# Performance work log

Hardware: AMD Instinct MI355X
Metric: run time of the kernel (lower is better)

The kernel has to match this reference:

```python
import jax, jax.numpy as jnp
import numpy as np

N_U = 50000
N_V = 50000
E = 640000
D = 128  # u_dim == v_dim == hid_dim (required for shape consistency)


def setup_inputs() -> dict:
    key = jax.random.key(0)
    ks = jax.random.split(key, 12)
    scale = 1.0 / np.sqrt(D)
    return {
        "X_u": jax.random.normal(ks[0], (N_U, D), dtype=jnp.float32),
        "X_v": jax.random.normal(ks[1], (N_V, D), dtype=jnp.float32),
        "edge_u": jax.random.randint(ks[2], (E,), 0, N_U, dtype=jnp.int32),
        "edge_v": jax.random.randint(ks[3], (E,), 0, N_V, dtype=jnp.int32),
        "W0": jax.random.uniform(ks[4], (D, D), jnp.float32, -scale, scale),
        "b0": jax.random.uniform(ks[5], (D,), jnp.float32, -scale, scale),
        "W1": jax.random.uniform(ks[6], (D, D), jnp.float32, -scale, scale),
        "b1": jax.random.uniform(ks[7], (D,), jnp.float32, -scale, scale),
        "W2": jax.random.uniform(ks[8], (D, D), jnp.float32, -scale, scale),
        "b2": jax.random.uniform(ks[9], (D,), jnp.float32, -scale, scale),
    }


def reference(X_u, X_v, edge_u, edge_v, W0, b0, W1, b1, W2, b2):
    # bipartite scatter-sum aggregations over the edge list
    def v2u(X):  # X: [N_V, D] -> [N_U, D]
        return jax.ops.segment_sum(X[edge_v], edge_u, num_segments=N_U)

    def u2v(X):  # X: [N_U, D] -> [N_V, D]
        return jax.ops.segment_sum(X[edge_u], edge_v, num_segments=N_V)

    # layer 0 (even): Linear(v_dim->hid) on X_v, then v2u sum
    last_X_u = v2u(X_v @ W0 + b0)
    # layer 1 (odd): Linear(u_dim->hid) on last_X_u, then u2v sum
    last_X_v = u2v(last_X_u @ W1 + b1)
    # layer 2 (even): Linear(v_dim->hid) on last_X_v, then v2u sum
    last_X_u = v2u(last_X_v @ W2 + b2)
    return last_X_u
```

## Files before the change

### kernel.cpp

```cpp
#include <hip/hip_runtime.h>

#define D 128
#define NROW 50000
#define NEDGE 640000
#define CAP 64

#define RBLK 160
#define EPB  4000
#define NBKT 196
#define CELL 64

typedef __attribute__((ext_vector_type(8))) short short8;
typedef __attribute__((ext_vector_type(4))) float f32x4;

__device__ __forceinline__ unsigned short f2bf(float f) {
    unsigned u = __float_as_uint(f);
    unsigned r = (u + 0x7fff + ((u >> 16) & 1)) >> 16;
    return (unsigned short)r;
}
__device__ __forceinline__ void acc2(float& e, float& o, unsigned g) {
    e += __uint_as_float(g << 16);
    o += __uint_as_float(g & 0xffff0000u);
}

__global__ __launch_bounds__(256) void route_cvt_gemm1(const int* __restrict__ eu,
                                                       const int* __restrict__ ev,
                                                       unsigned int* __restrict__ recbuf_u,
                                                       int* __restrict__ counts_u,
                                                       unsigned int* __restrict__ recbuf_v,
                                                       int* __restrict__ counts_v,
                                                       const float4* __restrict__ Xv4,
                                                       ushort4* __restrict__ Xb4,
                                                       const float* __restrict__ W0,
                                                       const float* __restrict__ b0,
                                                       const float* __restrict__ b1,
                                                       const float* __restrict__ W1,
                                                       float* __restrict__ T) {
    const int blk = blockIdx.x, tid = threadIdx.x;
    if (blk < 65) {
        __shared__ float R[2][128];
        int sub = tid >> 7, j = tid & 127;
        int i = blk * 2 + sub;
        bool valid = (i < 130);
        const float* row = nullptr;
        if (valid && i < 128) row = W0 + i * D;
        else if (valid && i == 128) row = b0;
        R[sub][j] = row ? row[j] : 0.f;
        __syncthreads();
        if (!valid) return;
        if (i == 129) { T[129 * D + j] = b1[j]; return; }
        float acc = 0.f;
#pragma unroll 8
        for (int k = 0; k < 128; k++) acc += R[sub][k] * W1[k * D + j];
        T[i * D + j] = acc;
    } else if (blk < 225) {
        __shared__ int cnt_s[NBKT];
        __shared__ unsigned int rec_s[NBKT * CELL];
        const int rblk = blk - 65;
        const int base = rblk * EPB;
        for (int dir = 0; dir < 2; dir++) {
            const int* __restrict__ kk = dir ? ev : eu;
            const int* __restrict__ pp = dir ? eu : ev;
            unsigned int* __restrict__ recbuf = dir ? recbuf_v : recbuf_u;
            int* __restrict__ counts = dir ? counts_v : counts_u;
            if (tid < NBKT) cnt_s[tid] = 0;
            __syncthreads();
            for (int e0 = tid; e0 < EPB; e0 += 256) {
                int e = base + e0;
                int key = kk[e], pay = pp[e];
                int k = key >> 8;
                int p = atomicAdd(&cnt_s[k], 1);
                if (p < CELL) rec_s[k * CELL + p] = ((unsigned)key << 16) | (unsigned)pay;
            }
            __syncthreads();
            if (tid < NBKT) {
                int c = cnt_s[tid];
                counts[rblk * NBKT + tid] = (c < CELL) ? c : CELL;
            }
            const int wave = tid >> 6, lane = tid & 63;
            for (int k = wave; k < NBKT; k += 4) {
                int c = cnt_s[k]; c = (c < CELL) ? c : CELL;
                if (lane < c)
                    recbuf[(size_t)(k * RBLK + rblk) * CELL + lane] = rec_s[k * CELL + lane];
            }
            __syncthreads();
        }
    } else {
        int i = (blk - 225) * 256 + tid;
        float4 v = Xv4[i];
        ushort4 o;
        o.x = f2bf(v.x); o.y = f2bf(v.y); o.z = f2bf(v.z); o.w = f2bf(v.w);
        Xb4[i] = o;
    }
}

__global__ __launch_bounds__(256) void ellbuild_sg2(const unsigned int* __restrict__ recbuf_u,
                                                    const int* __restrict__ counts_u,
                                                    const unsigned int* __restrict__ recbuf_v,
                                                    const int* __restrict__ counts_v,
                                                    unsigned short* __restrict__ ell_u,
                                                    int* __restrict__ cnt_u,
                                                    unsigned short* __restrict__ ell_v,
                                                    int* __restrict__ cnt_v,
                                                    const float* __restrict__ T,
                                                    const float* __restrict__ W2,
                                                    float* __restrict__ P,
                                                    unsigned short* __restrict__ PbT) {
    const int blk = blockIdx.x, tid = threadIdx.x;
    if (blk < 2 * NBKT) {
        const int dir = (blk >= NBKT) ? 1 : 0;
        const int k = dir ? blk - NBKT : blk;
        const unsigned int* __restrict__ recbuf = dir ? recbuf_v : recbuf_u;
        const int* __restrict__ counts = dir ? counts_v : counts_u;
        unsigned short* __restrict__ ell = dir ? ell_v : ell_u;
        int* __restrict__ cnt = dir ? cnt_v : cnt_u;

        __shared__ __align__(16) unsigned short ell_s[256 * CAP];
        __shared__ int cnt_s[256];
        __shared__ int seg_c[RBLK];
        cnt_s[tid] = 0;
        if (tid < RBLK) seg_c[tid] = counts[tid * NBKT + k];
        __syncthreads();

        const int wave = tid >> 6, lane = tid & 63;
        const unsigned int* rb = recbuf + (size_t)k * RBLK * CELL;
        int b = wave;
        int c0 = seg_c[b];
        unsigned int r0 = 0;
        if (lane < c0) r0 = rb[b * CELL + lane];
        while (b < RBLK) {
            int bn = b + 4;
            int c1 = 0; unsigned int r1 = 0;
            if (bn < RBLK) { c1 = seg_c[bn]; if (lane < c1) r1 = rb[bn * CELL + lane]; }
            if (lane < c0) {
                int lr = (r0 >> 16) & 255;
                int p = atomicAdd(&cnt_s[lr], 1);
                if (p < CAP) ell_s[lr * CAP + p] = (unsigned short)(r0 & 0xffff);
            }
            b = bn; c0 = c1; r0 = r1;
        }
        __syncthreads();
        const int row0 = k << 8;
        const int nrows = (row0 + 256 <= NROW) ? 256 : (NROW - row0);
        const uint4* src = (const uint4*)ell_s;
        uint4* dst = (uint4*)(ell + (size_t)row0 * CAP);
        for (int i = tid; i < nrows * 8; i += 256) dst[i] = src[i];
        if (tid < nrows) cnt[row0 + tid] = cnt_s[tid];
    } else {
        __shared__ float R[2][128];
        int idx = blk - 2 * NBKT;
        int sub = tid >> 7, j = tid & 127;
        int i = idx * 2 + sub;
        bool valid = (i < 130);
        R[sub][j] = valid ? T[i * D + j] : 0.f;
        __syncthreads();
        if (!valid) return;
        float acc = 0.f;
#pragma unroll 8
        for (int kk = 0; kk < 128; kk++) acc += R[sub][kk] * W2[kk * D + j];
        P[i * D + j] = acc;
        if (i < 128) PbT[j * 128 + i] = f2bf(acc);
    }
}

__device__ __forceinline__ uint4 gather_chunk(const unsigned short* __restrict__ Ac,
                                              const unsigned short* __restrict__ idx,
                                              int n) {
    float a0 = 0.f, a1 = 0.f, a2 = 0.f, a3 = 0.f, a4 = 0.f, a5 = 0.f, a6 = 0.f, a7 = 0.f;
    int i = 0;
    for (; i + 8 <= n; i += 8) {
        uint4 iv = *(const uint4*)(idx + i);
        uint4 q0 = *(const uint4*)(Ac + (size_t)(iv.x & 0xffffu) * D);
        uint4 q1 = *(const uint4*)(Ac + (size_t)(iv.x >> 16) * D);
        uint4 q2 = *(const uint4*)(Ac + (size_t)(iv.y & 0xffffu) * D);
        uint4 q3 = *(const uint4*)(Ac + (size_t)(iv.y >> 16) * D);
        uint4 q4 = *(const uint4*)(Ac + (size_t)(iv.z & 0xffffu) * D);
        uint4 q5 = *(const uint4*)(Ac + (size_t)(iv.z >> 16) * D);
        uint4 q6 = *(const uint4*)(Ac + (size_t)(iv.w & 0xffffu) * D);
        uint4 q7 = *(const uint4*)(Ac + (size_t)(iv.w >> 16) * D);
        acc2(a0, a1, q0.x); acc2(a2, a3, q0.y); acc2(a4, a5, q0.z); acc2(a6, a7, q0.w);
        acc2(a0, a1, q1.x); acc2(a2, a3, q1.y); acc2(a4, a5, q1.z); acc2(a6, a7, q1.w);
        acc2(a0, a1, q2.x); acc2(a2, a3, q2.y); acc2(a4, a5, q2.z); acc2(a6, a7, q2.w);
        acc2(a0, a1, q3.x); acc2(a2, a3, q3.y); acc2(a4, a5, q3.z); acc2(a6, a7, q3.w);
        acc2(a0, a1, q4.x); acc2(a2, a3, q4.y); acc2(a4, a5, q4.z); acc2(a6, a7, q4.w);
        acc2(a0, a1, q5.x); acc2(a2, a3, q5.y); acc2(a4, a5, q5.z); acc2(a6, a7, q5.w);
        acc2(a0, a1, q6.x); acc2(a2, a3, q6.y); acc2(a4, a5, q6.z); acc2(a6, a7, q6.w);
        acc2(a0, a1, q7.x); acc2(a2, a3, q7.y); acc2(a4, a5, q7.z); acc2(a6, a7, q7.w);
    }
    if (i + 4 <= n) {
        uint2 iv = *(const uint2*)(idx + i);
        uint4 q0 = *(const uint4*)(Ac + (size_t)(iv.x & 0xffffu) * D);
        uint4 q1 = *(const uint4*)(Ac + (size_t)(iv.x >> 16) * D);
        uint4 q2 = *(const uint4*)(Ac + (size_t)(iv.y & 0xffffu) * D);
        uint4 q3 = *(const uint4*)(Ac + (size_t)(iv.y >> 16) * D);
        acc2(a0, a1, q0.x); acc2(a2, a3, q0.y); acc2(a4, a5, q0.z); acc2(a6, a7, q0.w);
        acc2(a0, a1, q1.x); acc2(a2, a3, q1.y); acc2(a4, a5, q1.z); acc2(a6, a7, q1.w);
        acc2(a0, a1, q2.x); acc2(a2, a3, q2.y); acc2(a4, a5, q2.z); acc2(a6, a7, q2.w);
        acc2(a0, a1, q3.x); acc2(a2, a3, q3.y); acc2(a4, a5, q3.z); acc2(a6, a7, q3.w);
        i += 4;
    }
    for (; i < n; i++) {
        uint4 q0 = *(const uint4*)(Ac + (size_t)idx[i] * D);
        acc2(a0, a1, q0.x); acc2(a2, a3, q0.y); acc2(a4, a5, q0.z); acc2(a6, a7, q0.w);
    }
    uint4 o;
    o.x = (unsigned)f2bf(a0) | ((unsigned)f2bf(a1) << 16);
    o.y = (unsigned)f2bf(a2) | ((unsigned)f2bf(a3) << 16);
    o.z = (unsigned)f2bf(a4) | ((unsigned)f2bf(a5) << 16);
    o.w = (unsigned)f2bf(a6) | ((unsigned)f2bf(a7) << 16);
    return o;
}

__device__ __forceinline__ void gather_body(const unsigned short* __restrict__ A,
                                            const int* __restrict__ cnt,
                                            const unsigned short* __restrict__ ell,
                                            unsigned short* __restrict__ OUTb,
                                            int blk) {
    const int r = blk * 16 + (threadIdx.x >> 4);
    const int c = threadIdx.x & 15;
    int n = cnt[r]; n = (n < CAP) ? n : CAP;
    uint4 o = gather_chunk(A + c * 8, ell + (size_t)r * CAP, n);
    *(uint4*)(OUTb + (size_t)r * D + c * 8) = o;
}

__device__ __forceinline__ void tk_body(const int* __restrict__ cnt_v,
                                        const unsigned short* __restrict__ ell_v,
                                        const int* __restrict__ cnt_u,
                                        int* __restrict__ t, int v) {
    if (v >= NROW) return;
    int n = cnt_v[v]; n = (n < CAP) ? n : CAP;
    const unsigned short* row = ell_v + (size_t)v * CAP;
    int s = 0;
    for (int i = 0; i < n; i += 8) {
        uint4 iv = *(const uint4*)(row + i);
        unsigned sx[8] = {iv.x & 0xffffu, iv.x >> 16, iv.y & 0xffffu, iv.y >> 16,
                          iv.z & 0xffffu, iv.z >> 16, iv.w & 0xffffu, iv.w >> 16};
#pragma unroll
        for (int j = 0; j < 8; j++) if (i + j < n) s += cnt_u[sx[j]];
    }
    t[v] = s;
}

__device__ __forceinline__ void g23_body(const int* __restrict__ cnt_u,
                                         const unsigned short* __restrict__ ell_u,
                                         const int* __restrict__ cnt_v,
                                         const int* __restrict__ t,
                                         int* __restrict__ g2, int* __restrict__ g3, int u) {
    if (u >= NROW) return;
    int n = cnt_u[u]; n = (n < CAP) ? n : CAP;
    const unsigned short* row = ell_u + (size_t)u * CAP;
    int a = 0, b = 0;
    for (int i = 0; i < n; i += 8) {
        uint4 iv = *(const uint4*)(row + i);
        unsigned sx[8] = {iv.x & 0xffffu, iv.x >> 16, iv.y & 0xffffu, iv.y >> 16,
                          iv.z & 0xffffu, iv.z >> 16, iv.w & 0xffffu, iv.w >> 16};
#pragma unroll
        for (int j = 0; j < 8; j++)
            if (i + j < n) { a += t[sx[j]]; b += cnt_v[sx[j]]; }
    }
    g2[u] = a;
    g3[u] = b;
}

__global__ __launch_bounds__(256) void gather1_tk(const unsigned short* __restrict__ A,
                                                  const int* __restrict__ cnt_u,
                                                  const unsigned short* __restrict__ ell_u,
                                                  unsigned short* __restrict__ OUTb,
                                                  const int* __restrict__ cnt_v,
                                                  const unsigned short* __restrict__ ell_v,
                                                  int* __restrict__ t) {
    if (blockIdx.x < 3125) gather_body(A, cnt_u, ell_u, OUTb, blockIdx.x);
    else tk_body(cnt_v, ell_v, cnt_u, t, (blockIdx.x - 3125) * 256 + threadIdx.x);
}

__global__ __launch_bounds__(256) void gather2_g23(const unsigned short* __restrict__ A,
                                                   const int* __restrict__ cnt_v,
                                                   const unsigned short* __restrict__ ell_v,
                                                   unsigned short* __restrict__ OUTb,
                                                   const int* __restrict__ cnt_u,
                                                   const unsigned short* __restrict__ ell_u,
                                                   const int* __restrict__ t,
                                                   int* __restrict__ g2, int* __restrict__ g3) {
    if (blockIdx.x < 3125) gather_body(A, cnt_v, ell_v, OUTb, blockIdx.x);
    else g23_body(cnt_u, ell_u, cnt_v, t, g2, g3, (blockIdx.x - 3125) * 256 + threadIdx.x);
}

#define LSTRIDE 136

__global__ __launch_bounds__(256) void gather3_gemm(const unsigned short* __restrict__ B2,
                                                    const int* __restrict__ cnt_u,
                                                    const unsigned short* __restrict__ ell_u,
                                                    const unsigned short* __restrict__ PbT,
                                                    const float* __restrict__ P,
                                                    const float* __restrict__ b2,
                                                    const int* __restrict__ g2,
                                                    const int* __restrict__ g3,
                                                    const int* __restrict__ du,
                                                    float* __restrict__ OUT) {
    __shared__ __align__(16) unsigned short Asm[64 * LSTRIDE];
    const int tid = threadIdx.x;
    const int m0blk = blockIdx.x * 64;

    const int c = tid & 15;
#pragma unroll 1
    for (int it = 0; it < 4; it++) {
        int rl = (tid >> 4) + it * 16;
        int r = m0blk + rl;
        uint4 o = {0u, 0u, 0u, 0u};
        if (r < NROW) {
            int n = cnt_u[r]; n = (n < CAP) ? n : CAP;
            o = gather_chunk(B2 + c * 8, ell_u + (size_t)r * CAP, n);
        }
        *(uint4*)(Asm + rl * LSTRIDE + c * 8) = o;
    }
    __syncthreads();

    const int wave = tid >> 6;
    const int lane = tid & 63;
    const int ml = lane & 15;
    const int quad = lane >> 4;
    const int m0 = m0blk + wave * 16;
    if (m0 >= NROW) return;

    const uint4* zr = (const uint4*)(Asm + (size_t)(wave * 16 + ml) * LSTRIDE);

    f32x4 acc[8];
#pragma unroll
    for (int nt = 0; nt < 8; nt++) acc[nt] = (f32x4){0.f, 0.f, 0.f, 0.f};

#pragma unroll
    for (int kc = 0; kc < 4; kc++) {
        short8 a = __builtin_bit_cast(short8, zr[kc * 4 + quad]);
#pragma unroll
        for (int nt = 0; nt < 8; nt++) {
            const uint4* br = (const uint4*)(PbT + (size_t)(nt * 16 + ml) * D);
            short8 b = __builtin_bit_cast(short8, br[kc * 4 + quad]);
            acc[nt] = __builtin_amdgcn_mfma_f32_16x16x32_bf16(a, b, acc[nt], 0, 0, 0);
        }
    }

    float sg2[4], sg3[4], sdu[4];
#pragma unroll
    for (int reg = 0; reg < 4; reg++) {
        int r = m0 + quad * 4 + reg;
        sg2[reg] = (float)g2[r];
        sg3[reg] = (float)g3[r];
        sdu[reg] = (float)du[r];
    }
    const float* c0 = P + 128 * D;
    const float* c1 = P + 129 * D;
#pragma unroll
    for (int nt = 0; nt < 8; nt++) {
        int col = nt * 16 + ml;
        float cc0 = c0[col], cc1 = c1[col], cb2 = b2[col];
#pragma unroll
        for (int reg = 0; reg < 4; reg++) {
            int r = m0 + quad * 4 + reg;
            OUT[(size_t)r * D + col] = acc[nt][reg] + sg2[reg] * cc0 + sg3[reg] * cc1 + sdu[reg] * cb2;
        }
    }
}

extern "C" void kernel_launch(void* const* d_in, const int* in_sizes, int n_in,
                              void* d_out, int out_size, void* d_ws, size_t ws_size,
                              hipStream_t stream) {
    const float* X_v = (const float*)d_in[1];
    const int* edge_u = (const int*)d_in[2];
    const int* edge_v = (const int*)d_in[3];
    const float* W0 = (const float*)d_in[4];
    const float* b0 = (const float*)d_in[5];
    const float* W1 = (const float*)d_in[6];
    const float* b1 = (const float*)d_in[7];
    const float* W2 = (const float*)d_in[8];
    const float* b2 = (const float*)d_in[9];

    char* w = (char*)d_ws;
    unsigned short* A = (unsigned short*)w;
    unsigned short* ell_u = (unsigned short*)(w + 12800000);
    unsigned short* ell_v = ell_u + (size_t)NROW * CAP;
    int* cnt_u = (int*)(ell_v + (size_t)NROW * CAP);
    int* cnt_v = cnt_u + NROW;
    int* tbuf  = cnt_v + NROW;
    int* g2    = tbuf + NROW;
    int* g3    = g2 + NROW;
    float* T   = (float*)(g3 + NROW);
    float* P   = T + 130 * D;
    unsigned short* PbT = (unsigned short*)(P + 130 * D);
    unsigned int* recbuf_u = (unsigned int*)(PbT + 128 * 128);
    unsigned int* recbuf_v = recbuf_u + (size_t)NBKT * RBLK * CELL;
    int* counts_u = (int*)(recbuf_v + (size_t)NBKT * RBLK * CELL);
    int* counts_v = counts_u + NBKT * RBLK;

    float* OUT = (float*)d_out;
    unsigned short* B1 = (unsigned short*)d_out;
    unsigned short* B2 = (unsigned short*)recbuf_u;
    const dim3 blk(256);

    route_cvt_gemm1<<<65 + RBLK + 6250, blk, 0, stream>>>(edge_u, edge_v,
                                                          recbuf_u, counts_u, recbuf_v, counts_v,
                                                          (const float4*)X_v, (ushort4*)B1,
                                                          W0, b0, b1, W1, T);
    ellbuild_sg2<<<2 * NBKT + 65, blk, 0, stream>>>(recbuf_u, counts_u, recbuf_v, counts_v,
                                                    ell_u, cnt_u, ell_v, cnt_v,
                                                    T, W2, P, PbT);
    gather1_tk<<<3125 + 196, blk, 0, stream>>>(B1, cnt_u, ell_u, A, cnt_v, ell_v, tbuf);
    gather2_g23<<<3125 + 196, blk, 0, stream>>>(A, cnt_v, ell_v, B2, cnt_u, ell_u, tbuf, g2, g3);
    gather3_gemm<<<782, blk, 0, stream>>>(B2, cnt_u, ell_u, PbT, P, b2, g2, g3, cnt_u, OUT);
}
```

Baseline: 261.2 us.

## Split final gather-GEMM into 16-row blocks with waves sharing rows across columns

The final gather+GEMM kernel now processes 16 rows per block instead of 64, with each of the four waves computing two 16-column tiles of the same 16 rows. The grid grows from 782 to 3125 blocks, so the latency-bound gather phase gets more parallelism and the LDS footprint per block shrinks, which raises occupancy. In exchange, each block does a quarter of the gather work, PbT is reread by more blocks, and bounds checks are removed on the assumption that the row count divides evenly by 16.

```diff
diff --git a/kernel.cpp b/kernel.cpp
--- a/kernel.cpp
+++ b/kernel.cpp
@@ -297,20 +297,16 @@
                                                     const int* __restrict__ g3,
                                                     const int* __restrict__ du,
                                                     float* __restrict__ OUT) {
-    __shared__ __align__(16) unsigned short Asm[64 * LSTRIDE];
+    __shared__ __align__(16) unsigned short Asm[16 * LSTRIDE];
     const int tid = threadIdx.x;
-    const int m0blk = blockIdx.x * 64;
-
-    const int c = tid & 15;
-#pragma unroll 1
-    for (int it = 0; it < 4; it++) {
-        int rl = (tid >> 4) + it * 16;
-        int r = m0blk + rl;
-        uint4 o = {0u, 0u, 0u, 0u};
-        if (r < NROW) {
-            int n = cnt_u[r]; n = (n < CAP) ? n : CAP;
-            o = gather_chunk(B2 + c * 8, ell_u + (size_t)r * CAP, n);
-        }
+    const int r0blk = blockIdx.x * 16;
+
+    {
+        const int rl = tid >> 4;
+        const int c = tid & 15;
+        int r = r0blk + rl;
+        int n = cnt_u[r]; n = (n < CAP) ? n : CAP;
+        uint4 o = gather_chunk(B2 + c * 8, ell_u + (size_t)r * CAP, n);
         *(uint4*)(Asm + rl * LSTRIDE + c * 8) = o;
     }
     __syncthreads();
@@ -319,30 +315,29 @@
     const int lane = tid & 63;
     const int ml = lane & 15;
     const int quad = lane >> 4;
-    const int m0 = m0blk + wave * 16;
-    if (m0 >= NROW) return;
-
-    const uint4* zr = (const uint4*)(Asm + (size_t)(wave * 16 + ml) * LSTRIDE);
-
-    f32x4 acc[8];
-#pragma unroll
-    for (int nt = 0; nt < 8; nt++) acc[nt] = (f32x4){0.f, 0.f, 0.f, 0.f};
+
+    const uint4* zr = (const uint4*)(Asm + (size_t)ml * LSTRIDE);
+
+    f32x4 acc[2];
+    acc[0] = (f32x4){0.f, 0.f, 0.f, 0.f};
+    acc[1] = (f32x4){0.f, 0.f, 0.f, 0.f};
 
 #pragma unroll
     for (int kc = 0; kc < 4; kc++) {
         short8 a = __builtin_bit_cast(short8, zr[kc * 4 + quad]);
 #pragma unroll
-        for (int nt = 0; nt < 8; nt++) {
+        for (int j = 0; j < 2; j++) {
+            int nt = wave * 2 + j;
             const uint4* br = (const uint4*)(PbT + (size_t)(nt * 16 + ml) * D);
             short8 b = __builtin_bit_cast(short8, br[kc * 4 + quad]);
-            acc[nt] = __builtin_amdgcn_mfma_f32_16x16x32_bf16(a, b, acc[nt], 0, 0, 0);
+            acc[j] = __builtin_amdgcn_mfma_f32_16x16x32_bf16(a, b, acc[j], 0, 0, 0);
         }
     }
 
     float sg2[4], sg3[4], sdu[4];
 #pragma unroll
     for (int reg = 0; reg < 4; reg++) {
-        int r = m0 + quad * 4 + reg;
+        int r = r0blk + quad * 4 + reg;
         sg2[reg] = (float)g2[r];
         sg3[reg] = (float)g3[r];
         sdu[reg] = (float)du[r];
@@ -350,13 +345,13 @@
     const float* c0 = P + 128 * D;
     const float* c1 = P + 129 * D;
 #pragma unroll
-    for (int nt = 0; nt < 8; nt++) {
-        int col = nt * 16 + ml;
+    for (int j = 0; j < 2; j++) {
+        int col = (wave * 2 + j) * 16 + ml;
         float cc0 = c0[col], cc1 = c1[col], cb2 = b2[col];
 #pragma unroll
         for (int reg = 0; reg < 4; reg++) {
-            int r = m0 + quad * 4 + reg;
-            OUT[(size_t)r * D + col] = acc[nt][reg] + sg2[reg] * cc0 + sg3[reg] * cc1 + sdu[reg] * cb2;
+            int r = r0blk + quad * 4 + reg;
+            OUT[(size_t)r * D + col] = acc[j][reg] + sg2[reg] * cc0 + sg3[reg] * cc1 + sdu[reg] * cb2;
         }
     }
 }
@@ -405,5 +400,5 @@
                                                     T, W2, P, PbT);
     gather1_tk<<<3125 + 196, blk, 0, stream>>>(B1, cnt_u, ell_u, A, cnt_v, ell_v, tbuf);
     gather2_g23<<<3125 + 196, blk, 0, stream>>>(A, cnt_v, ell_v, B2, cnt_u, ell_u, tbuf, g2, g3);
-    gather3_gemm<<<782, blk, 0, stream>>>(B2, cnt_u, ell_u, PbT, P, b2, g2, g3, cnt_u, OUT);
-}
+    gather3_gemm<<<3125, blk, 0, stream>>>(B2, cnt_u, ell_u, PbT, P, b2, g2, g3, cnt_u, OUT);
+}
```

New measurement: 247.1 us. 5.4% less time.
